# Kernel tuning notes

Hardware: AMD Instinct MI355X
Metric: run time of the kernel (lower is better)

Reference implementation:

```python
import jax, jax.numpy as jnp
import numpy as np

N_NODES = 100000
N_EDGES = 1200000
F_IN, F_HID, F_OUT = 64, 16, 40


def setup_inputs() -> dict:
    key = jax.random.key(0)
    ks = jax.random.split(key, 6)
    x = jax.random.normal(ks[0], (N_NODES, F_IN), dtype=jnp.float32)
    edge_index = jax.random.randint(ks[1], (2, N_EDGES), 0, N_NODES, dtype=jnp.int32)
    s1 = 1.0 / np.sqrt(F_IN)
    s2 = 1.0 / np.sqrt(F_HID)
    return {
        "x": x,
        "edge_index": edge_index,
        "W1_self": jax.random.normal(ks[2], (F_IN, F_HID), dtype=jnp.float32) * s1,
        "W1_neigh": jax.random.normal(ks[3], (F_IN, F_HID), dtype=jnp.float32) * s1,
        "b1": jnp.zeros((F_HID,), dtype=jnp.float32),
        "W2_self": jax.random.normal(ks[4], (F_HID, F_OUT), dtype=jnp.float32) * s2,
        "W2_neigh": jax.random.normal(ks[5], (F_HID, F_OUT), dtype=jnp.float32) * s2,
        "b2": jnp.zeros((F_OUT,), dtype=jnp.float32),
    }


def _sage_conv(x, src, dst, W_self, W_neigh, b):
    # gather source features along edges, mean-aggregate onto destinations
    n = x.shape[0]
    deg = jax.ops.segment_sum(jnp.ones((src.shape[0],), x.dtype), dst, num_segments=n)
    agg = jax.ops.segment_sum(x[src], dst, num_segments=n)
    agg = agg / jnp.maximum(deg, 1.0)[:, None]
    return x @ W_self + agg @ W_neigh + b


def reference(x, edge_index, W1_self, W1_neigh, b1, W2_self, W2_neigh, b2):
    src, dst = edge_index[0], edge_index[1]
    h = jax.nn.relu(_sage_conv(x, src, dst, W1_self, W1_neigh, b1))
    # F.dropout with training=False is identity (eval-mode reference)
    out = _sage_conv(h, src, dst, W2_self, W2_neigh, b2)
    return jax.nn.log_softmax(out, axis=1)
```

## Files before the change

kernel.cpp:

```cpp
#include <hip/hip_runtime.h>
#include <math.h>

#define N_NODES 100000
#define N_EDGES 1200000
#define F_IN    64
#define F_HID   16
#define F_OUT   40

#define BK_SHIFT 7
#define BK_NODES 128
#define NB 782
#define CAP 1792
#define S1_EPB 4096
#define BIN_BLOCKS ((N_EDGES + S1_EPB - 1) / S1_EPB)
#define GEMM_BLOCKS ((N_NODES + 15) / 16)

typedef _Float16 v2h __attribute__((ext_vector_type(2)));

__global__ __launch_bounds__(256)
void k1_bin_gemm(const int* __restrict__ src, const int* __restrict__ dst,
                 unsigned* __restrict__ cursor, unsigned* __restrict__ csr,
                 const float* __restrict__ x, const float* __restrict__ Wn,
                 const float* __restrict__ Ws, const float* __restrict__ b1,
                 _Float16* __restrict__ t1, _Float16* __restrict__ xs, int nE) {
    __shared__ __align__(16) char smem[12416];
    int tid = threadIdx.x;
    int bid = blockIdx.x;
    if (bid < BIN_BLOCKS) {
        unsigned* cnt = (unsigned*)smem;
        for (int i = tid; i < NB; i += 256) cnt[i] = 0u;
        __syncthreads();
        int tb = bid * S1_EPB + tid * 16;
        if (tb + 16 <= nE) {
            const int4* d4 = (const int4*)(dst + tb);
#pragma unroll
            for (int j = 0; j < 4; j++) {
                int4 v = d4[j];
                atomicAdd(&cnt[((unsigned)v.x) >> BK_SHIFT], 1u);
                atomicAdd(&cnt[((unsigned)v.y) >> BK_SHIFT], 1u);
                atomicAdd(&cnt[((unsigned)v.z) >> BK_SHIFT], 1u);
                atomicAdd(&cnt[((unsigned)v.w) >> BK_SHIFT], 1u);
            }
        } else {
            for (int e = tb; e < nE && e < tb + 16; e++)
                atomicAdd(&cnt[((unsigned)dst[e]) >> BK_SHIFT], 1u);
        }
        __syncthreads();
        for (int i = tid; i < NB; i += 256) {
            unsigned c = cnt[i];
            cnt[i] = c ? atomicAdd(&cursor[i], c) : 0u;
        }
        __syncthreads();
        if (tb + 16 <= nE) {
            const int4* d4 = (const int4*)(dst + tb);
            const int4* s4 = (const int4*)(src + tb);
#pragma unroll
            for (int j = 0; j < 4; j++) {
                int4 dv = d4[j];
                int4 sv = s4[j];
                int da[4] = {dv.x, dv.y, dv.z, dv.w};
                int sa[4] = {sv.x, sv.y, sv.z, sv.w};
#pragma unroll
                for (int q = 0; q < 4; q++) {
                    unsigned d = (unsigned)da[q];
                    unsigned b = d >> BK_SHIFT;
                    unsigned pos = atomicAdd(&cnt[b], 1u);
                    if (pos < CAP)
                        csr[b * CAP + pos] = (((unsigned)sa[q]) << BK_SHIFT) | (d & (BK_NODES - 1));
                }
            }
        } else {
            for (int e = tb; e < nE && e < tb + 16; e++) {
                unsigned d = (unsigned)dst[e];
                unsigned b = d >> BK_SHIFT;
                unsigned pos = atomicAdd(&cnt[b], 1u);
                if (pos < CAP)
                    csr[b * CAP + pos] = (((unsigned)src[e]) << BK_SHIFT) | (d & (BK_NODES - 1));
            }
        }
    } else {
        float* sWn = (float*)smem;
        float* sWs = sWn + 1024;
        float* sb  = sWs + 1024;
        float* sx  = sb + 16;
        for (int i = tid; i < F_IN * F_HID; i += 256) { sWn[i] = Wn[i]; sWs[i] = Ws[i]; }
        if (tid < F_HID) sb[tid] = b1[tid];
        int row0 = (bid - BIN_BLOCKS) * 16;
        const float* xg = x + (size_t)row0 * F_IN;
        for (int i = tid; i < 16 * F_IN; i += 256)
            sx[(i >> 6) * 65 + (i & 63)] = xg[i];
        __syncthreads();
        int r = tid >> 4, c = tid & 15;
        int row = row0 + r;
        const float* xr = sx + r * 65;
        float sn = 0.f, ss = sb[c];
#pragma unroll
        for (int k = 0; k < F_IN; k++) {
            float xv = xr[k];
            sn += xv * sWn[k * F_HID + c];
            ss += xv * sWs[k * F_HID + c];
        }
        t1[row * F_HID + c] = (_Float16)sn;
        xs[row * F_HID + c] = (_Float16)ss;
    }
}

__global__ __launch_bounds__(512)
void k2_sort_agg1(const unsigned* __restrict__ cursor, unsigned* __restrict__ csr,
                  unsigned* __restrict__ node_info,
                  const _Float16* __restrict__ t1, _Float16* __restrict__ xsh) {
    __shared__ unsigned words[CAP];
    __shared__ unsigned sorted[CAP];
    __shared__ unsigned hist[BK_NODES];
    __shared__ unsigned lcur[BK_NODES];
    __shared__ unsigned begs[BK_NODES];
    int tid = threadIdx.x;
    int b = blockIdx.x;
    unsigned count = cursor[b]; if (count > CAP) count = CAP;
    unsigned* reg = csr + (size_t)b * CAP;
    for (unsigned i = tid; i < count; i += 512) words[i] = reg[i];
    if (tid < BK_NODES) hist[tid] = 0u;
    __syncthreads();
    for (unsigned i = tid; i < count; i += 512)
        atomicAdd(&hist[words[i] & (BK_NODES - 1)], 1u);
    __syncthreads();
    unsigned hv = (tid < BK_NODES) ? hist[tid] : 0u;
    __syncthreads();
    for (int d = 1; d < BK_NODES; d <<= 1) {
        unsigned t = (tid < BK_NODES && tid >= d) ? hist[tid - d] : 0u;
        __syncthreads();
        if (tid < BK_NODES) hist[tid] += t;
        __syncthreads();
    }
    if (tid < BK_NODES) {
        unsigned excl = hist[tid] - hv;
        begs[tid] = excl;
        lcur[tid] = excl;
        int node = (b << BK_SHIFT) + tid;
        if (node < N_NODES) node_info[node] = (excl << 16) | hv;
    }
    __syncthreads();
    for (unsigned i = tid; i < count; i += 512) {
        unsigned w = words[i];
        unsigned pos = atomicAdd(&lcur[w & (BK_NODES - 1)], 1u);
        sorted[pos] = w >> BK_SHIFT;
    }
    __syncthreads();
    for (unsigned i = tid; i < count; i += 512) reg[i] = sorted[i];

    int grp = tid >> 3;
    int f = tid & 7;
    const v2h* t2 = (const v2h*)t1;
#pragma unroll
    for (int half = 0; half < 2; half++) {
        int ln = grp + half * 64;
        int node = (b << BK_SHIFT) + ln;
        if (node >= N_NODES) continue;
        unsigned beg = begs[ln];
        unsigned end = lcur[ln];
        float ax = 0.f, ay = 0.f;
        unsigned e = beg;
        for (; e + 4 <= end; e += 4) {
            unsigned s0 = sorted[e], s1 = sorted[e + 1];
            unsigned s2 = sorted[e + 2], s3 = sorted[e + 3];
            v2h v0 = t2[s0 * 8 + f], v1 = t2[s1 * 8 + f];
            v2h v2 = t2[s2 * 8 + f], v3 = t2[s3 * 8 + f];
            ax += (float)v0.x + (float)v1.x + (float)v2.x + (float)v3.x;
            ay += (float)v0.y + (float)v1.y + (float)v2.y + (float)v3.y;
        }
        for (; e < end; e++) {
            v2h v = t2[sorted[e] * 8 + f];
            ax += (float)v.x; ay += (float)v.y;
        }
        float inv = 1.0f / fmaxf((float)(end - beg), 1.0f);
        int g = node * 8 + f;
        v2h xv = ((const v2h*)xsh)[g];
        v2h hvv;
        hvv.x = (_Float16)fmaxf((float)xv.x + ax * inv, 0.f);
        hvv.y = (_Float16)fmaxf((float)xv.y + ay * inv, 0.f);
        ((v2h*)xsh)[g] = hvv;
    }
}

__global__ __launch_bounds__(256)
void agg2_kernel(const unsigned* __restrict__ node_info, const unsigned* __restrict__ csr,
                 const _Float16* __restrict__ h,
                 const float* __restrict__ Ws, const float* __restrict__ Wn,
                 const float* __restrict__ b2, float* __restrict__ out, int n) {
    __shared__ float sWs[F_HID * F_OUT];
    __shared__ float sWn[F_HID * F_OUT];
    __shared__ float sb[F_OUT];
    int tid = threadIdx.x;
    for (int i = tid; i < F_HID * F_OUT; i += 256) { sWs[i] = Ws[i]; sWn[i] = Wn[i]; }
    if (tid < F_OUT) sb[tid] = b2[tid];
    __syncthreads();
    int g = blockIdx.x * 256 + tid;
    int node = g >> 3;
    int f = g & 7;
    if (node >= n) return;
    unsigned info = node_info[node];
    int beg = (node >> BK_SHIFT) * CAP + (int)(info >> 16);
    int cnt = (int)(info & 0xFFFFu);
    int end = beg + cnt;
    const v2h* h2 = (const v2h*)h;
    float ax = 0.f, ay = 0.f;
    int e = beg;
    for (; e + 4 <= end; e += 4) {
        unsigned s0 = csr[e], s1 = csr[e + 1], s2 = csr[e + 2], s3 = csr[e + 3];
        v2h v0 = h2[s0 * 8 + f], v1 = h2[s1 * 8 + f];
        v2h v2 = h2[s2 * 8 + f], v3 = h2[s3 * 8 + f];
        ax += (float)v0.x + (float)v1.x + (float)v2.x + (float)v3.x;
        ay += (float)v0.y + (float)v1.y + (float)v2.y + (float)v3.y;
    }
    for (; e < end; e++) {
        v2h v = h2[csr[e] * 8 + f];
        ax += (float)v.x; ay += (float)v.y;
    }
    float inv = 1.0f / fmaxf((float)cnt, 1.0f);
    ax *= inv; ay *= inv;
    v2h hs = h2[g];
    float hx = (float)hs.x, hy = (float)hs.y;
    float arow[F_HID], hrow[F_HID];
#pragma unroll
    for (int k = 0; k < 8; k++) {
        arow[2 * k]     = __shfl(ax, k, 8);
        arow[2 * k + 1] = __shfl(ay, k, 8);
        hrow[2 * k]     = __shfl(hx, k, 8);
        hrow[2 * k + 1] = __shfl(hy, k, 8);
    }
    float logit[5];
    float m = -INFINITY;
#pragma unroll
    for (int j = 0; j < 5; j++) {
        int c = j * 8 + f;
        float s = sb[c];
#pragma unroll
        for (int k = 0; k < F_HID; k++)
            s += hrow[k] * sWs[k * F_OUT + c] + arow[k] * sWn[k * F_OUT + c];
        logit[j] = s;
        m = fmaxf(m, s);
    }
    m = fmaxf(m, __shfl_xor(m, 1, 8));
    m = fmaxf(m, __shfl_xor(m, 2, 8));
    m = fmaxf(m, __shfl_xor(m, 4, 8));
    float sum = 0.f;
#pragma unroll
    for (int j = 0; j < 5; j++) sum += __expf(logit[j] - m);
    sum += __shfl_xor(sum, 1, 8);
    sum += __shfl_xor(sum, 2, 8);
    sum += __shfl_xor(sum, 4, 8);
    float lse = m + __logf(sum);
#pragma unroll
    for (int j = 0; j < 5; j++)
        out[node * F_OUT + j * 8 + f] = logit[j] - lse;
}

extern "C" void kernel_launch(void* const* d_in, const int* in_sizes, int n_in,
                              void* d_out, int out_size, void* d_ws, size_t ws_size,
                              hipStream_t stream) {
    const float* x        = (const float*)d_in[0];
    const int*   edges    = (const int*)d_in[1];
    const float* W1_self  = (const float*)d_in[2];
    const float* W1_neigh = (const float*)d_in[3];
    const float* b1       = (const float*)d_in[4];
    const float* W2_self  = (const float*)d_in[5];
    const float* W2_neigh = (const float*)d_in[6];
    const float* b2       = (const float*)d_in[7];
    float* out = (float*)d_out;

    const int* src = edges;
    const int* dst = edges + N_EDGES;

    char* base = (char*)d_ws;
    unsigned* cursor    = (unsigned*)base;
    unsigned* node_info = (unsigned*)(base + 4096);
    unsigned* csr       = (unsigned*)(base + 404608);
    _Float16* t1        = (_Float16*)(base + 6009984);
    _Float16* xsh       = (_Float16*)(base + 9209984);

    hipMemsetAsync(cursor, 0, 4096, stream);

    k1_bin_gemm<<<BIN_BLOCKS + GEMM_BLOCKS, 256, 0, stream>>>(
        src, dst, cursor, csr, x, W1_neigh, W1_self, b1, t1, xsh, N_EDGES);
    k2_sort_agg1<<<NB, 512, 0, stream>>>(cursor, csr, node_info, t1, xsh);
    agg2_kernel<<<(N_NODES * 8) / 256, 256, 0, stream>>>(node_info, csr, xsh,
                                                         W2_self, W2_neigh, b2, out, N_NODES);
}
```

Baseline: 159.6 us.

## Use MFMA fp16 for layer-1 GEMM and halve edge-binning block size

Replaces the scalar LDS-based layer-1 projection with MFMA 16x16x32 fp16 instructions. Each wave keeps the weights in registers and handles two 16-row tiles, reading x straight from global memory. The binning blocks now process 2048 edges instead of 4096, giving more blocks for parallelism. The bucket capacity is raised to a power of two so indexing uses shifts, and the workspace offsets are realigned. Inputs and weights are converted to fp16 before the multiply, which may change precision slightly; the larger CAP also increases csr workspace use.

```diff
diff --git a/kernel.cpp b/kernel.cpp
--- a/kernel.cpp
+++ b/kernel.cpp
@@ -10,12 +10,16 @@
 #define BK_SHIFT 7
 #define BK_NODES 128
 #define NB 782
-#define CAP 1792
-#define S1_EPB 4096
+#define CAP 2048
+#define CAP_SHIFT 11
+#define S1_EPB 2048
 #define BIN_BLOCKS ((N_EDGES + S1_EPB - 1) / S1_EPB)
-#define GEMM_BLOCKS ((N_NODES + 15) / 16)
-
-typedef _Float16 v2h __attribute__((ext_vector_type(2)));
+#define N_TILES ((N_NODES + 15) / 16)
+#define GEMM_BLOCKS ((N_TILES + 7) / 8)
+
+typedef _Float16 v2h  __attribute__((ext_vector_type(2)));
+typedef _Float16 v8hf __attribute__((ext_vector_type(8)));
+typedef float    vf4  __attribute__((ext_vector_type(4)));
 
 __global__ __launch_bounds__(256)
 void k1_bin_gemm(const int* __restrict__ src, const int* __restrict__ dst,
@@ -23,18 +27,17 @@
                  const float* __restrict__ x, const float* __restrict__ Wn,
                  const float* __restrict__ Ws, const float* __restrict__ b1,
                  _Float16* __restrict__ t1, _Float16* __restrict__ xs, int nE) {
-    __shared__ __align__(16) char smem[12416];
+    __shared__ unsigned cnt[NB];
     int tid = threadIdx.x;
     int bid = blockIdx.x;
     if (bid < BIN_BLOCKS) {
-        unsigned* cnt = (unsigned*)smem;
         for (int i = tid; i < NB; i += 256) cnt[i] = 0u;
         __syncthreads();
-        int tb = bid * S1_EPB + tid * 16;
-        if (tb + 16 <= nE) {
+        int tb = bid * S1_EPB + tid * 8;
+        if (tb + 8 <= nE) {
             const int4* d4 = (const int4*)(dst + tb);
 #pragma unroll
-            for (int j = 0; j < 4; j++) {
+            for (int j = 0; j < 2; j++) {
                 int4 v = d4[j];
                 atomicAdd(&cnt[((unsigned)v.x) >> BK_SHIFT], 1u);
                 atomicAdd(&cnt[((unsigned)v.y) >> BK_SHIFT], 1u);
@@ -42,7 +45,7 @@
                 atomicAdd(&cnt[((unsigned)v.w) >> BK_SHIFT], 1u);
             }
         } else {
-            for (int e = tb; e < nE && e < tb + 16; e++)
+            for (int e = tb; e < nE && e < tb + 8; e++)
                 atomicAdd(&cnt[((unsigned)dst[e]) >> BK_SHIFT], 1u);
         }
         __syncthreads();
@@ -51,11 +54,11 @@
             cnt[i] = c ? atomicAdd(&cursor[i], c) : 0u;
         }
         __syncthreads();
-        if (tb + 16 <= nE) {
+        if (tb + 8 <= nE) {
             const int4* d4 = (const int4*)(dst + tb);
             const int4* s4 = (const int4*)(src + tb);
 #pragma unroll
-            for (int j = 0; j < 4; j++) {
+            for (int j = 0; j < 2; j++) {
                 int4 dv = d4[j];
                 int4 sv = s4[j];
                 int da[4] = {dv.x, dv.y, dv.z, dv.w};
@@ -66,42 +69,67 @@
                     unsigned b = d >> BK_SHIFT;
                     unsigned pos = atomicAdd(&cnt[b], 1u);
                     if (pos < CAP)
-                        csr[b * CAP + pos] = (((unsigned)sa[q]) << BK_SHIFT) | (d & (BK_NODES - 1));
+                        csr[(b << CAP_SHIFT) + pos] = (((unsigned)sa[q]) << BK_SHIFT) | (d & (BK_NODES - 1));
                 }
             }
         } else {
-            for (int e = tb; e < nE && e < tb + 16; e++) {
+            for (int e = tb; e < nE && e < tb + 8; e++) {
                 unsigned d = (unsigned)dst[e];
                 unsigned b = d >> BK_SHIFT;
                 unsigned pos = atomicAdd(&cnt[b], 1u);
                 if (pos < CAP)
-                    csr[b * CAP + pos] = (((unsigned)src[e]) << BK_SHIFT) | (d & (BK_NODES - 1));
+                    csr[(b << CAP_SHIFT) + pos] = (((unsigned)src[e]) << BK_SHIFT) | (d & (BK_NODES - 1));
             }
         }
     } else {
-        float* sWn = (float*)smem;
-        float* sWs = sWn + 1024;
-        float* sb  = sWs + 1024;
-        float* sx  = sb + 16;
-        for (int i = tid; i < F_IN * F_HID; i += 256) { sWn[i] = Wn[i]; sWs[i] = Ws[i]; }
-        if (tid < F_HID) sb[tid] = b1[tid];
-        int row0 = (bid - BIN_BLOCKS) * 16;
-        const float* xg = x + (size_t)row0 * F_IN;
-        for (int i = tid; i < 16 * F_IN; i += 256)
-            sx[(i >> 6) * 65 + (i & 63)] = xg[i];
-        __syncthreads();
-        int r = tid >> 4, c = tid & 15;
-        int row = row0 + r;
-        const float* xr = sx + r * 65;
-        float sn = 0.f, ss = sb[c];
-#pragma unroll
-        for (int k = 0; k < F_IN; k++) {
-            float xv = xr[k];
-            sn += xv * sWn[k * F_HID + c];
-            ss += xv * sWs[k * F_HID + c];
-        }
-        t1[row * F_HID + c] = (_Float16)sn;
-        xs[row * F_HID + c] = (_Float16)ss;
+        int wv = tid >> 6;
+        int lane = tid & 63;
+        int mrow = lane & 15;
+        int quad = lane >> 4;
+        int col = mrow;
+        v8hf bn0, bn1, bs0, bs1;
+#pragma unroll
+        for (int j = 0; j < 8; j++) {
+            int k0 = quad * 8 + j;
+            bn0[j] = (_Float16)Wn[k0 * F_HID + col];
+            bs0[j] = (_Float16)Ws[k0 * F_HID + col];
+            bn1[j] = (_Float16)Wn[(k0 + 32) * F_HID + col];
+            bs1[j] = (_Float16)Ws[(k0 + 32) * F_HID + col];
+        }
+        float bias = b1[col];
+        int gw = (bid - BIN_BLOCKS) * 4 + wv;
+#pragma unroll
+        for (int t = 0; t < 2; t++) {
+            int tile = gw * 2 + t;
+            if (tile >= N_TILES) break;
+            int row0 = tile * 16;
+            const float* xr = x + (size_t)(row0 + mrow) * F_IN;
+            float4 x0 = *(const float4*)(xr + quad * 8);
+            float4 x1 = *(const float4*)(xr + quad * 8 + 4);
+            float4 x2 = *(const float4*)(xr + 32 + quad * 8);
+            float4 x3 = *(const float4*)(xr + 32 + quad * 8 + 4);
+            v8hf a0, a1;
+            a0[0] = (_Float16)x0.x; a0[1] = (_Float16)x0.y;
+            a0[2] = (_Float16)x0.z; a0[3] = (_Float16)x0.w;
+            a0[4] = (_Float16)x1.x; a0[5] = (_Float16)x1.y;
+            a0[6] = (_Float16)x1.z; a0[7] = (_Float16)x1.w;
+            a1[0] = (_Float16)x2.x; a1[1] = (_Float16)x2.y;
+            a1[2] = (_Float16)x2.z; a1[3] = (_Float16)x2.w;
+            a1[4] = (_Float16)x3.x; a1[5] = (_Float16)x3.y;
+            a1[6] = (_Float16)x3.z; a1[7] = (_Float16)x3.w;
+            vf4 accn = {0.f, 0.f, 0.f, 0.f};
+            vf4 accs = {bias, bias, bias, bias};
+            accn = __builtin_amdgcn_mfma_f32_16x16x32_f16(a0, bn0, accn, 0, 0, 0);
+            accn = __builtin_amdgcn_mfma_f32_16x16x32_f16(a1, bn1, accn, 0, 0, 0);
+            accs = __builtin_amdgcn_mfma_f32_16x16x32_f16(a0, bs0, accs, 0, 0, 0);
+            accs = __builtin_amdgcn_mfma_f32_16x16x32_f16(a1, bs1, accs, 0, 0, 0);
+#pragma unroll
+            for (int r = 0; r < 4; r++) {
+                int row = row0 + quad * 4 + r;
+                t1[row * F_HID + col] = (_Float16)accn[r];
+                xs[row * F_HID + col] = (_Float16)accs[r];
+            }
+        }
     }
 }
 
@@ -117,7 +145,7 @@
     int tid = threadIdx.x;
     int b = blockIdx.x;
     unsigned count = cursor[b]; if (count > CAP) count = CAP;
-    unsigned* reg = csr + (size_t)b * CAP;
+    unsigned* reg = csr + ((size_t)b << CAP_SHIFT);
     for (unsigned i = tid; i < count; i += 512) words[i] = reg[i];
     if (tid < BK_NODES) hist[tid] = 0u;
     __syncthreads();
@@ -199,7 +227,7 @@
     int f = g & 7;
     if (node >= n) return;
     unsigned info = node_info[node];
-    int beg = (node >> BK_SHIFT) * CAP + (int)(info >> 16);
+    int beg = ((node >> BK_SHIFT) << CAP_SHIFT) + (int)(info >> 16);
     int cnt = (int)(info & 0xFFFFu);
     int end = beg + cnt;
     const v2h* h2 = (const v2h*)h;
@@ -273,10 +301,10 @@
 
     char* base = (char*)d_ws;
     unsigned* cursor    = (unsigned*)base;
-    unsigned* node_info = (unsigned*)(base + 4096);
-    unsigned* csr       = (unsigned*)(base + 404608);
-    _Float16* t1        = (_Float16*)(base + 6009984);
-    _Float16* xsh       = (_Float16*)(base + 9209984);
+    unsigned* node_info = (unsigned*)(base + (1u << 20));
+    unsigned* csr       = (unsigned*)(base + (2u << 20));
+    _Float16* t1        = (_Float16*)(base + (16u << 20));
+    _Float16* xsh       = (_Float16*)(base + (24u << 20));
 
     hipMemsetAsync(cursor, 0, 4096, stream);
 
```

Result: slower. 165.9 us (+4.0%).
